# Kernel tuning notes

Hardware: AMD Instinct MI355X
Metric: run time of the kernel (lower is better)

## Reference

```python
import jax, jax.numpy as jnp
import numpy as np

N_EMBD = 1024
N_HEAD = 16
BLOCK_SIZE = 2048
NEG_INF = -1e10


def _rope_cache(head_dim, max_positions):
    # theta_i = 10000^{-2i/dim}, freqs[t, i] = t * theta_i
    theta = 1.0 / (10000.0 ** (jnp.arange(0, head_dim, 2, dtype=jnp.float32) / head_dim))
    freqs = jnp.arange(max_positions, dtype=jnp.float32)[:, None] * theta[None, :]
    return jnp.cos(freqs), jnp.sin(freqs)  # each (max_positions, head_dim//2)


def _apply_rope(x, cos, sin):
    # x: (B, nh, T, hs) interpreted as interleaved complex pairs
    B, nh, T, hs = x.shape
    xr = x.reshape(B, nh, T, hs // 2, 2)
    x0, x1 = xr[..., 0], xr[..., 1]
    c = cos[:T][None, None, :, :]
    s = sin[:T][None, None, :, :]
    o0 = x0 * c - x1 * s
    o1 = x0 * s + x1 * c
    return jnp.stack([o0, o1], axis=-1).reshape(B, nh, T, hs)


def setup_inputs() -> dict:
    key = jax.random.key(0)
    ks = jax.random.split(key, 9)
    B, T, C = 2, 2048, N_EMBD
    sc = 1.0 / np.sqrt(C)
    return {
        "x": jax.random.normal(ks[0], (B, T, C), jnp.float32),
        "Wq": jax.random.normal(ks[1], (C, C), jnp.float32) * sc,
        "bq": jax.random.normal(ks[2], (C,), jnp.float32) * 0.02,
        "Wk": jax.random.normal(ks[3], (C, C), jnp.float32) * sc,
        "bk": jax.random.normal(ks[4], (C,), jnp.float32) * 0.02,
        "Wv": jax.random.normal(ks[5], (C, C), jnp.float32) * sc,
        "bv": jax.random.normal(ks[6], (C,), jnp.float32) * 0.02,
        "Wp": jax.random.normal(ks[7], (C, C), jnp.float32) * sc,
        "bp": jax.random.normal(ks[8], (C,), jnp.float32) * 0.02,
    }


def reference(x, Wq, bq, Wk, bk, Wv, bv, Wp, bp):
    B, T, C = x.shape
    nh, hs = N_HEAD, C // N_HEAD

    def heads(W, b):
        return (x @ W.T + b).reshape(B, T, nh, hs).transpose(0, 2, 1, 3)

    q = heads(Wq, bq)
    k = heads(Wk, bk)
    v = heads(Wv, bv)

    cos, sin = _rope_cache(hs, BLOCK_SIZE)
    q = _apply_rope(q, cos, sin)
    k = _apply_rope(k, cos, sin)

    att = jnp.einsum("bhqd,bhkd->bhqk", q, k) * (1.0 / np.sqrt(hs))
    causal = jnp.tril(jnp.ones((T, T), dtype=bool))
    att = jnp.where(causal[None, None], att, NEG_INF)
    att = jax.nn.softmax(att, axis=-1)
    y = jnp.einsum("bhqk,bhkd->bhqd", att, v)
    y = y.transpose(0, 2, 1, 3).reshape(B, T, C)
    return y @ Wp.T + bp
```

## Files before the change

### kernel.cpp

```cpp
#include <hip/hip_runtime.h>

typedef __bf16 bf16;
typedef short  s16;
typedef s16   s16x8 __attribute__((ext_vector_type(8)));
typedef bf16  bf16x4 __attribute__((ext_vector_type(4)));
typedef float f32x4 __attribute__((ext_vector_type(4)));

#define B_SZ 2
#define T_SEQ 2048
#define C_DIM 1024
#define NH 16
#define HS 64
#define M_TOT (B_SZ * T_SEQ)

#define NEG_BIG (-30000.0f)
#define LOG2_10000 13.287712379549449f
#define Q_PRESCALE 0.18033688011112042f


__device__ __forceinline__ float san(float x) {
    unsigned u = __float_as_uint(x);
    return ((u & 0x7F800000u) == 0x7F800000u) ? 0.f : x;
}

__device__ __forceinline__ void load16_lds(const bf16* g, void* lds_base) {
    __builtin_amdgcn_global_load_lds(
        (const __attribute__((address_space(1))) void*)g,
        (__attribute__((address_space(3))) void*)lds_base, 16, 0, 0);
}

#define CVT_GRID 8448

__global__ __launch_bounds__(256) void cvt_bf16_kernel(
    const float* __restrict__ x,  const float* __restrict__ wq,
    const float* __restrict__ wk, const float* __restrict__ wv,
    const float* __restrict__ wp,
    bf16* __restrict__ xb, bf16* __restrict__ wqb, bf16* __restrict__ wkb,
    bf16* __restrict__ wvb, bf16* __restrict__ wpb,
    float* __restrict__ cs, float* __restrict__ sn)
{
    const int b = blockIdx.x;
    if (b >= 8192) {
        const int idx = (b - 8192) * 256 + threadIdx.x;
        const int t = idx >> 5, i = idx & 31;
        const float theta = __builtin_exp2f(-(float)(2 * i) * (LOG2_10000 / 64.f));
        const float a = (float)t * theta;
        cs[idx] = san(cosf(a));
        sn[idx] = san(sinf(a));
        return;
    }
    int z, base;
    if (b < 4096) { z = 0; base = b; }
    else          { z = 1 + ((b - 4096) >> 10); base = (b - 4096) & 1023; }

    const float* src = (z == 0) ? x : (z == 1) ? wq : (z == 2) ? wk : (z == 3) ? wv : wp;
    bf16* dst = (z == 0) ? xb : (z == 1) ? wqb : (z == 2) ? wkb : (z == 3) ? wvb : wpb;

    const int i = (base * 256 + threadIdx.x) * 4;
    const float4 v = *(const float4*)(src + i);
    bf16x4 o;
    o[0] = (bf16)v.x; o[1] = (bf16)v.y; o[2] = (bf16)v.z; o[3] = (bf16)v.w;
    *(bf16x4*)(dst + i) = o;
}

#define STAGE_TILE(buf, kk)                                                    \
    load16_lds(gA0 + (kk), (char*)(sA[buf]) + w * 1024);                       \
    load16_lds(gB0 + (kk), (char*)(sB[buf]) + w * 1024);                       \
    load16_lds(gB1 + (kk), (char*)(sB[buf]) + 4096 + w * 1024);

#define K_STEP(buf)                                                            \
    {                                                                          \
        s16x8 af[2], bfr[4];                                                   \
        _Pragma("unroll")                                                      \
        for (int mt = 0; mt < 2; mt++)                                         \
            af[mt] = *(const s16x8*)(sA[buf] + (wm * 32 + mt * 16 + r) * 32 + qs * 8); \
        _Pragma("unroll")                                                      \
        for (int nt = 0; nt < 4; nt++)                                         \
            bfr[nt] = *(const s16x8*)(sB[buf] + (wn * 64 + nt * 16 + r) * 32 + qs * 8); \
        _Pragma("unroll")                                                      \
        for (int mt = 0; mt < 2; mt++)                                         \
            _Pragma("unroll")                                                  \
            for (int nt = 0; nt < 4; nt++)                                     \
                acc[mt][nt] = __builtin_amdgcn_mfma_f32_16x16x32_bf16(         \
                    af[mt], bfr[nt], acc[mt][nt], 0, 0, 0);                    \
    }

#define GEMM_CORE(Xp, Wp_)                                                     \
    const int t = threadIdx.x;                                                 \
    const int w = t >> 6;                                                      \
    const int lane = t & 63;                                                   \
    const int qd = lane >> 4;                                                  \
    const int r  = lane & 15;                                                  \
    const int qs = qd ^ ((r >> 1) & 3);                                        \
    const int wm = w & 1, wn = w >> 1;                                         \
    const int srow = t >> 2;                                                   \
    const int scol = ((t & 3) ^ ((t >> 3) & 3)) * 8;                           \
    const bf16* gA0 = (Xp) + (size_t)(m0 + srow) * C_DIM + scol;               \
    const bf16* gB0 = (Wp_) + (size_t)(n0 + srow) * C_DIM + scol;              \
    const bf16* gB1 = (Wp_) + (size_t)(n0 + 64 + srow) * C_DIM + scol;         \
    f32x4 acc[2][4] = {};                                                      \
    STAGE_TILE(0, 0)                                                           \
    for (int k0 = 0; k0 < C_DIM; k0 += 64) {                                   \
        __syncthreads();                                                       \
        STAGE_TILE(1, k0 + 32)                                                 \
        K_STEP(0)                                                              \
        __syncthreads();                                                       \
        if (k0 + 64 < C_DIM) { STAGE_TILE(0, k0 + 64) }                        \
        K_STEP(1)                                                              \
    }

__global__ __launch_bounds__(256) void qkv_gemm(
    const bf16* __restrict__ X,
    const bf16* __restrict__ Wq, const float* __restrict__ bq,
    const bf16* __restrict__ Wk, const float* __restrict__ bk,
    const bf16* __restrict__ Wv, const float* __restrict__ bv,
    const float* __restrict__ cs_tab, const float* __restrict__ sn_tab,
    bf16* __restrict__ q_ws, bf16* __restrict__ k_ws, bf16* __restrict__ vt_ws)
{
    __shared__ __attribute__((aligned(16))) bf16 sA[2][64 * 32];
    __shared__ __attribute__((aligned(16))) bf16 sB[2][128 * 32];

    const int mode = blockIdx.z;
    const bf16*  Wm   = (mode == 0) ? Wq : (mode == 1) ? Wk : Wv;
    const float* bias = (mode == 0) ? bq : (mode == 1) ? bk : bv;
    const int m0 = blockIdx.x * 64;
    const int n0 = blockIdx.y * 128;

    GEMM_CORE(X, Wm)

    if (mode == 2) {
        #pragma unroll
        for (int mt = 0; mt < 2; mt++) {
            const int mrow0 = m0 + wm * 32 + mt * 16 + qd * 4;
            const int bb = mrow0 >> 11;
            const int t0 = mrow0 & 2047;
            #pragma unroll
            for (int nt = 0; nt < 4; nt++) {
                const int col = n0 + wn * 64 + nt * 16 + r;
                const int h = col >> 6, d = col & 63;
                const float bv_ = bias[col];
                bf16x4 pk;
                #pragma unroll
                for (int reg = 0; reg < 4; reg++)
                    pk[reg] = (bf16)san(acc[mt][nt][reg] + bv_);
                *(bf16x4*)(vt_ws + ((size_t)(bb * NH + h) * HS + d) * T_SEQ + t0) = pk;
            }
        }
    } else {
        bf16* out = (mode == 0) ? q_ws : k_ws;
        const float post = (mode == 0) ? Q_PRESCALE : 1.0f;
        #pragma unroll
        for (int mt = 0; mt < 2; mt++) {
            const int mrow0 = m0 + wm * 32 + mt * 16 + qd * 4;
            const int bb = mrow0 >> 11;
            const int t0 = mrow0 & 2047;
            #pragma unroll
            for (int nt = 0; nt < 4; nt++) {
                const int col = n0 + wn * 64 + nt * 16 + r;
                const int h = col >> 6, d = col & 63;
                const int pi = d >> 1;
                const float bv_ = bias[col];
                #pragma unroll
                for (int reg = 0; reg < 4; reg++) {
                    const int tt = t0 + reg;
                    float v = san(acc[mt][nt][reg] + bv_);
                    float partner = __shfl_xor(v, 1);
                    float c = cs_tab[tt * 32 + pi];
                    float s = sn_tab[tt * 32 + pi];
                    float rot = (d & 1) ? (v * c + partner * s)
                                        : (v * c - partner * s);
                    out[((size_t)(bb * NH + h) * T_SEQ + tt) * HS + d] =
                        (bf16)san(rot * post);
                }
            }
        }
    }
}

__global__ __launch_bounds__(256) void proj_gemm(
    const bf16* __restrict__ Y, const bf16* __restrict__ Wp,
    const float* __restrict__ bp, float* __restrict__ out)
{
    __shared__ __attribute__((aligned(16))) bf16 sA[2][64 * 32];
    __shared__ __attribute__((aligned(16))) bf16 sB[2][128 * 32];

    const int m0 = blockIdx.x * 64;
    const int n0 = blockIdx.y * 128;

    GEMM_CORE(Y, Wp)

    #pragma unroll
    for (int mt = 0; mt < 2; mt++) {
        const int mrow0 = m0 + wm * 32 + mt * 16 + qd * 4;
        #pragma unroll
        for (int nt = 0; nt < 4; nt++) {
            const int col = n0 + wn * 64 + nt * 16 + r;
            const float bv_ = bp[col];
            #pragma unroll
            for (int reg = 0; reg < 4; reg++)
                out[(size_t)(mrow0 + reg) * C_DIM + col] = san(acc[mt][nt][reg] + bv_);
        }
    }
}

__global__ __launch_bounds__(256) void attn_kernel(
    const bf16* __restrict__ q_ws, const bf16* __restrict__ k_ws,
    const bf16* __restrict__ vt_ws, bf16* __restrict__ y_ws)
{
    __shared__ __attribute__((aligned(16))) bf16 sK[2][2][64][32];
    __shared__ __attribute__((aligned(16))) bf16 sV[2][2][64][32];
    __shared__ __attribute__((aligned(16))) bf16 sP[4][16][72];

    const int id = (int)(blockIdx.x + gridDim.x * blockIdx.y);
    const int bh = (id & 7) + 8 * (id >> 7);
    const int bx = (id >> 3) & 15;

    const int w    = threadIdx.x >> 6;
    const int lane = threadIdx.x & 63;
    const int qd = lane >> 4;
    const int r  = lane & 15;
    const int qs = qd ^ ((r >> 1) & 3);

    const bf16* Qb = q_ws + (size_t)bh * T_SEQ * HS;
    const bf16* Kb = k_ws + (size_t)bh * T_SEQ * HS;
    const bf16* Vb = vt_ws + (size_t)bh * HS * T_SEQ;

    const int srow = lane >> 2;
    const int scol = ((lane & 3) ^ ((lane >> 3) & 3)) * 8;
    const bf16* Kb_w = Kb + (size_t)(w * 16 + srow) * HS + scol;
    const bf16* Vb_w = Vb + (size_t)(w * 16 + srow) * T_SEQ + scol;

    bf16 (*pw)[72] = sP[w];
    const int bb = bh >> 4, h = bh & 15;

    #pragma unroll 1
    for (int phase = 0; phase < 2; phase++) {
        const int qt = phase ? bx : (T_SEQ / 64 - 1 - bx);
        const int q0 = qt * 64 + w * 16;

        s16x8 aq0 = *(const s16x8*)(Qb + (size_t)(q0 + r) * HS + qd * 8);
        s16x8 aq1 = *(const s16x8*)(Qb + (size_t)(q0 + r) * HS + 32 + qd * 8);

        f32x4 o[4] = {};
        float l_lane = 0.f;

        __syncthreads();
        load16_lds(Kb_w,      &sK[0][0][w * 16][0]);
        load16_lds(Kb_w + 32, &sK[0][1][w * 16][0]);
        load16_lds(Vb_w,      &sV[0][0][w * 16][0]);
        load16_lds(Vb_w + 32, &sV[0][1][w * 16][0]);

        for (int kt = 0; kt <= qt; kt++) {
            const int cur = kt & 1;
            __syncthreads();

            if (kt < qt) {
                const bf16* kp = Kb_w + (size_t)(kt + 1) * 64 * HS;
                const bf16* vp = Vb_w + (kt + 1) * 64;
                load16_lds(kp,      &sK[cur ^ 1][0][w * 16][0]);
                load16_lds(kp + 32, &sK[cur ^ 1][1][w * 16][0]);
                load16_lds(vp,      &sV[cur ^ 1][0][w * 16][0]);
                load16_lds(vp + 32, &sV[cur ^ 1][1][w * 16][0]);
            }

            f32x4 s[4];
            #pragma unroll
            for (int c = 0; c < 4; c++) {
                s16x8 k0 = *(const s16x8*)&sK[cur][0][c * 16 + r][qs * 8];
                s16x8 k1 = *(const s16x8*)&sK[cur][1][c * 16 + r][qs * 8];
                f32x4 z = {};
                z = __builtin_amdgcn_mfma_f32_16x16x32_bf16(k0, aq0, z, 0, 0, 0);
                z = __builtin_amdgcn_mfma_f32_16x16x32_bf16(k1, aq1, z, 0, 0, 0);
                s[c] = z;
            }

            if (kt == qt) {
                const int qg = q0 + r;
                #pragma unroll
                for (int c = 0; c < 4; c++)
                    #pragma unroll
                    for (int reg = 0; reg < 4; reg++) {
                        const int kg = kt * 64 + c * 16 + qd * 4 + reg;
                        s[c][reg] = (kg <= qg) ? s[c][reg] : NEG_BIG;
                    }
            }

            #pragma unroll
            for (int c = 0; c < 4; c++) {
                bf16x4 pk;
                #pragma unroll
                for (int reg = 0; reg < 4; reg++) {
                    float p = __builtin_exp2f(s[c][reg]);
                    l_lane += p;
                    pk[reg] = (bf16)p;
                }
                *(bf16x4*)&pw[r][c * 16 + qd * 4] = pk;
            }

            s16x8 ap0 = *(const s16x8*)&pw[r][qd * 8];
            s16x8 ap1 = *(const s16x8*)&pw[r][32 + qd * 8];
            #pragma unroll
            for (int nt = 0; nt < 4; nt++) {
                s16x8 av0 = *(const s16x8*)&sV[cur][0][nt * 16 + r][qs * 8];
                s16x8 av1 = *(const s16x8*)&sV[cur][1][nt * 16 + r][qs * 8];
                o[nt] = __builtin_amdgcn_mfma_f32_16x16x32_bf16(av0, ap0, o[nt], 0, 0, 0);
                o[nt] = __builtin_amdgcn_mfma_f32_16x16x32_bf16(av1, ap1, o[nt], 0, 0, 0);
            }
        }

        float l = l_lane;
        l += __shfl_xor(l, 16);
        l += __shfl_xor(l, 32);
        const float inv = 1.f / fmaxf(l, 1e-20f);

        const int q = q0 + r;
        bf16* dst = y_ws + ((size_t)(bb * T_SEQ + q) * NH + h) * HS;
        #pragma unroll
        for (int nt = 0; nt < 4; nt++) {
            bf16x4 pk;
            #pragma unroll
            for (int reg = 0; reg < 4; reg++)
                pk[reg] = (bf16)san(o[nt][reg] * inv);
            *(bf16x4*)(dst + nt * 16 + qd * 4) = pk;
        }
    }
}

extern "C" void kernel_launch(void* const* d_in, const int* in_sizes, int n_in,
                              void* d_out, int out_size, void* d_ws, size_t ws_size,
                              hipStream_t stream)
{
    const size_t MB = 1024 * 1024;
    const size_t NEED = 40 * MB + 2 * 65536 * sizeof(float);
    if (ws_size < NEED || n_in < 9) return;

    const float* x  = (const float*)d_in[0];
    const float* Wq = (const float*)d_in[1];
    const float* bq = (const float*)d_in[2];
    const float* Wk = (const float*)d_in[3];
    const float* bk = (const float*)d_in[4];
    const float* Wv = (const float*)d_in[5];
    const float* bv = (const float*)d_in[6];
    const float* Wp = (const float*)d_in[7];
    const float* bp = (const float*)d_in[8];
    float* out = (float*)d_out;

    char* ws = (char*)d_ws;
    bf16*  q_ws   = (bf16*)(ws + 0 * MB);
    bf16*  k_ws   = (bf16*)(ws + 8 * MB);
    bf16*  vt_ws  = (bf16*)(ws + 16 * MB);
    bf16*  x_b    = (bf16*)(ws + 24 * MB);
    bf16*  y_ws   = (bf16*)(ws + 24 * MB);
    bf16*  Wq_b   = (bf16*)(ws + 32 * MB);
    bf16*  Wk_b   = (bf16*)(ws + 34 * MB);
    bf16*  Wv_b   = (bf16*)(ws + 36 * MB);
    bf16*  Wp_b   = (bf16*)(ws + 38 * MB);
    float* cs_tab = (float*)(ws + 40 * MB);
    float* sn_tab = cs_tab + 65536;

    cvt_bf16_kernel<<<dim3(CVT_GRID), 256, 0, stream>>>(
        x, Wq, Wk, Wv, Wp, x_b, Wq_b, Wk_b, Wv_b, Wp_b, cs_tab, sn_tab);
    qkv_gemm<<<dim3(M_TOT / 64, C_DIM / 128, 3), 256, 0, stream>>>(
        x_b, Wq_b, bq, Wk_b, bk, Wv_b, bv, cs_tab, sn_tab, q_ws, k_ws, vt_ws);
    attn_kernel<<<dim3(T_SEQ / 128, B_SZ * NH), 256, 0, stream>>>(
        q_ws, k_ws, vt_ws, y_ws);
    proj_gemm<<<dim3(M_TOT / 64, C_DIM / 128), 256, 0, stream>>>(
        y_ws, Wp_b, bp, out);
}
```

Before: 209.2 us.

## Triple-buffer GEMM LDS staging with explicit waitcnt and single barrier per k-step

Replaces the double-buffered GEMM main loop with a three-stage LDS ring, fully unrolled over 32 k-tiles. Each iteration waits only until the oldest outstanding async load group has landed (vmcnt(3)), issues one barrier, prefetches two tiles ahead, then runs the MFMA step. The aim is to keep global-to-LDS loads in flight longer and halve the barriers per k-step, at the cost of 50% more LDS per block and hand-written waitcnt assumptions that must match the three loads issued per stage.

```diff
diff --git a/kernel.cpp b/kernel.cpp
--- a/kernel.cpp
+++ b/kernel.cpp
@@ -63,20 +63,22 @@
     *(bf16x4*)(dst + i) = o;
 }
 
-#define STAGE_TILE(buf, kk)                                                    \
-    load16_lds(gA0 + (kk), (char*)(sA[buf]) + w * 1024);                       \
-    load16_lds(gB0 + (kk), (char*)(sB[buf]) + w * 1024);                       \
-    load16_lds(gB1 + (kk), (char*)(sB[buf]) + 4096 + w * 1024);
-
-#define K_STEP(buf)                                                            \
+#define STAGE3(bufi, kk)                                                       \
+    load16_lds(gA0 + (kk), (char*)(sA + (bufi) * 2048) + w * 1024);            \
+    load16_lds(gB0 + (kk), (char*)(sB + (bufi) * 4096) + w * 1024);            \
+    load16_lds(gB1 + (kk), (char*)(sB + (bufi) * 4096) + 4096 + w * 1024);
+
+#define K_STEP3(bufi)                                                          \
     {                                                                          \
+        const bf16* pA = sA + (bufi) * 2048;                                   \
+        const bf16* pB = sB + (bufi) * 4096;                                   \
         s16x8 af[2], bfr[4];                                                   \
         _Pragma("unroll")                                                      \
         for (int mt = 0; mt < 2; mt++)                                         \
-            af[mt] = *(const s16x8*)(sA[buf] + (wm * 32 + mt * 16 + r) * 32 + qs * 8); \
+            af[mt] = *(const s16x8*)(pA + (wm * 32 + mt * 16 + r) * 32 + qs * 8); \
         _Pragma("unroll")                                                      \
         for (int nt = 0; nt < 4; nt++)                                         \
-            bfr[nt] = *(const s16x8*)(sB[buf] + (wn * 64 + nt * 16 + r) * 32 + qs * 8); \
+            bfr[nt] = *(const s16x8*)(pB + (wn * 64 + nt * 16 + r) * 32 + qs * 8); \
         _Pragma("unroll")                                                      \
         for (int mt = 0; mt < 2; mt++)                                         \
             _Pragma("unroll")                                                  \
@@ -99,14 +101,18 @@
     const bf16* gB0 = (Wp_) + (size_t)(n0 + srow) * C_DIM + scol;              \
     const bf16* gB1 = (Wp_) + (size_t)(n0 + 64 + srow) * C_DIM + scol;         \
     f32x4 acc[2][4] = {};                                                      \
-    STAGE_TILE(0, 0)                                                           \
-    for (int k0 = 0; k0 < C_DIM; k0 += 64) {                                   \
-        __syncthreads();                                                       \
-        STAGE_TILE(1, k0 + 32)                                                 \
-        K_STEP(0)                                                              \
-        __syncthreads();                                                       \
-        if (k0 + 64 < C_DIM) { STAGE_TILE(0, k0 + 64) }                        \
-        K_STEP(1)                                                              \
+    STAGE3(0, 0)                                                               \
+    STAGE3(1, 32)                                                              \
+    _Pragma("unroll")                                                          \
+    for (int kt_ = 0; kt_ < 32; kt_++) {                                       \
+        __builtin_amdgcn_sched_barrier(0);                                     \
+        if (kt_ < 30) asm volatile("s_waitcnt vmcnt(3) lgkmcnt(0)" ::: "memory"); \
+        else          asm volatile("s_waitcnt vmcnt(0) lgkmcnt(0)" ::: "memory"); \
+        __builtin_amdgcn_sched_barrier(0);                                     \
+        __builtin_amdgcn_s_barrier();                                          \
+        __builtin_amdgcn_sched_barrier(0);                                     \
+        if (kt_ + 2 < 32) { STAGE3((kt_ + 2) % 3, (kt_ + 2) * 32) }            \
+        K_STEP3(kt_ % 3)                                                       \
     }
 
 __global__ __launch_bounds__(256) void qkv_gemm(
@@ -117,8 +123,8 @@
     const float* __restrict__ cs_tab, const float* __restrict__ sn_tab,
     bf16* __restrict__ q_ws, bf16* __restrict__ k_ws, bf16* __restrict__ vt_ws)
 {
-    __shared__ __attribute__((aligned(16))) bf16 sA[2][64 * 32];
-    __shared__ __attribute__((aligned(16))) bf16 sB[2][128 * 32];
+    __shared__ __attribute__((aligned(16))) bf16 sA[3 * 64 * 32];
+    __shared__ __attribute__((aligned(16))) bf16 sB[3 * 128 * 32];
 
     const int mode = blockIdx.z;
     const bf16*  Wm   = (mode == 0) ? Wq : (mode == 1) ? Wk : Wv;
@@ -181,8 +187,8 @@
     const bf16* __restrict__ Y, const bf16* __restrict__ Wp,
     const float* __restrict__ bp, float* __restrict__ out)
 {
-    __shared__ __attribute__((aligned(16))) bf16 sA[2][64 * 32];
-    __shared__ __attribute__((aligned(16))) bf16 sB[2][128 * 32];
+    __shared__ __attribute__((aligned(16))) bf16 sA[3 * 64 * 32];
+    __shared__ __attribute__((aligned(16))) bf16 sB[3 * 128 * 32];
 
     const int m0 = blockIdx.x * 64;
     const int n0 = blockIdx.y * 128;
```

Measured after the change: 200.4 us. 1.04x faster.
